# Kernel tuning notes

Hardware: AMD Instinct MI355X
Metric: run time of the kernel (lower is better)

Reference implementation:

```python
import jax, jax.numpy as jnp
import numpy as np

B, T, D = 2, 2048, 1024
N_HEADS, N_KV_HEADS = 16, 4
D_HEAD = D // N_HEADS            # 64
N_GROUPS = N_HEADS // N_KV_HEADS  # 4
ROPE_THETA = 10000.0


def _rope_freqs(t, d_head, theta):
    inv = 1.0 / (theta ** (jnp.arange(0, d_head, 2, dtype=jnp.float32) / d_head))  # (d_head/2,)
    ang = jnp.arange(t, dtype=jnp.float32)[:, None] * inv[None, :]                 # (T, d_head/2)
    return jnp.stack([jnp.cos(ang), jnp.sin(ang)], axis=-1)                        # (T, d_head/2, 2)


def _apply_rope(x, freqs):
    # x: (B, T, H, d_head); freqs: (T, d_head/2, 2) = (cos, sin)
    xr = x.reshape(*x.shape[:-1], -1, 2)          # (B,T,H,d/2,2)
    xre, xim = xr[..., 0], xr[..., 1]
    fre = freqs[None, :, None, :, 0]              # (1,T,1,d/2)
    fim = freqs[None, :, None, :, 1]
    outre = xre * fre - xim * fim
    outim = xre * fim + xim * fre
    return jnp.stack([outre, outim], axis=-1).reshape(x.shape)


def setup_inputs() -> dict:
    key = jax.random.key(0)
    ks = jax.random.split(key, 5)
    x = jax.random.normal(ks[0], (B, T, D), dtype=jnp.float32)
    w_q = jax.random.normal(ks[1], (N_HEADS * D_HEAD, D), dtype=jnp.float32) * 0.02
    w_k = jax.random.normal(ks[2], (N_KV_HEADS * D_HEAD, D), dtype=jnp.float32) * 0.02
    w_v = jax.random.normal(ks[3], (N_KV_HEADS * D_HEAD, D), dtype=jnp.float32) * 0.02
    w_o = jax.random.normal(ks[4], (D, N_HEADS * D_HEAD), dtype=jnp.float32) * 0.02
    rope_freqs = _rope_freqs(T, D_HEAD, ROPE_THETA)
    causal = jnp.tril(jnp.ones((T, T), dtype=bool))
    mask = jnp.where(causal, 0.0, -1e9).astype(jnp.float32)[None, None]  # (1,1,T,T)
    return {"x": x, "rope_freqs": rope_freqs, "mask": mask,
            "w_q": w_q, "w_k": w_k, "w_v": w_v, "w_o": w_o}


def reference(x, rope_freqs, mask, w_q, w_k, w_v, w_o):
    # projections (torch Linear: y = x @ W.T)
    q = jnp.einsum('btd,od->bto', x, w_q).reshape(B, T, N_HEADS, D_HEAD)
    k = jnp.einsum('btd,od->bto', x, w_k).reshape(B, T, N_KV_HEADS, D_HEAD)
    v = jnp.einsum('btd,od->bto', x, w_v).reshape(B, T, N_KV_HEADS, D_HEAD)
    q = _apply_rope(q, rope_freqs)
    k = _apply_rope(k, rope_freqs)
    # GQA: expand KV heads (kv head h -> N_GROUPS contiguous query heads)
    k = jnp.repeat(k, N_GROUPS, axis=2)   # (B,T,H,d)
    v = jnp.repeat(v, N_GROUPS, axis=2)
    q = q.transpose(0, 2, 1, 3)           # (B,H,T,d)
    k = k.transpose(0, 2, 1, 3)
    v = v.transpose(0, 2, 1, 3)
    scale = 1.0 / np.sqrt(D_HEAD).astype(np.float32)
    scores = jnp.einsum('bhqd,bhkd->bhqk', q, k) * scale + mask
    attn = jax.nn.softmax(scores, axis=-1)
    out = jnp.einsum('bhqk,bhkd->bhqd', attn, v)
    out = out.transpose(0, 2, 1, 3).reshape(B, T, N_HEADS * D_HEAD)
    return jnp.einsum('bto,do->btd', out, w_o)
```

## Files before the change

kernel.cpp:

```cpp
#include <hip/hip_runtime.h>
#include <hip/hip_bf16.h>
#include <cstddef>

#define TT   2048
#define NH   16
#define NKV  4
#define DH   64

typedef __bf16 bf16x8 __attribute__((ext_vector_type(8)));
typedef float  f32x4  __attribute__((ext_vector_type(4)));

#if __has_builtin(__builtin_amdgcn_exp2f)
#define EXP2F(x) __builtin_amdgcn_exp2f(x)
#else
#define EXP2F(x) __expf((x) * 0.69314718056f)
#endif

#define QSCALE 0.180336880f

__global__ __launch_bounds__(256)
void cast_kernel(const float* __restrict__ x,  const float* __restrict__ wq,
                 const float* __restrict__ wk, const float* __restrict__ wv,
                 const float* __restrict__ wo,
                 __bf16* __restrict__ xb, __bf16* __restrict__ wqkv,
                 __bf16* __restrict__ wob)
{
    const int g = blockIdx.x * 256 + threadIdx.x;
    const float* src;
    __bf16* dst;
    int off;
    if (g < 1048576)       { src = x;  dst = xb;   off = g; }
    else if (g < 1310720)  { src = wq; dst = wqkv; off = g - 1048576; }
    else if (g < 1376256)  { src = wk; dst = wqkv + 1048576; off = g - 1310720; }
    else if (g < 1441792)  { src = wv; dst = wqkv + 1310720; off = g - 1376256; }
    else                   { src = wo; dst = wob;  off = g - 1441792; }
    const float4 v = *(const float4*)(src + (size_t)off * 4);
    union { __bf16 h[4]; uint2 u; } o;
    o.h[0] = (__bf16)v.x; o.h[1] = (__bf16)v.y;
    o.h[2] = (__bf16)v.z; o.h[3] = (__bf16)v.w;
    *(uint2*)(dst + (size_t)off * 4) = o.u;
}

template<int MODE>
__global__ __launch_bounds__(128, 2)
void mm_kernel(const __bf16* __restrict__ A,
               const __bf16* __restrict__ W,
               const float* __restrict__ rope,
               void* __restrict__ O0, void* __restrict__ O1,
               void* __restrict__ O2)
{
    constexpr int K  = 1024;
    constexpr int NK = K / 32;
    __shared__ __bf16 As[64 * 32];
    __shared__ __bf16 Bs[128 * 32];

    const int tid  = threadIdx.x;
    const int lane = tid & 63;
    const int wv   = tid >> 6;
    const int quad = lane >> 4;
    const int lc   = lane & 15;
    const int gm0  = blockIdx.y * 64;
    const int gn0  = blockIdx.x * 128;
    const int wc0  = wv * 64;

    size_t gaA[2], gaB[4];
    int lsA[2], lsB[4];
#pragma unroll
    for (int j = 0; j < 2; j++) {
        const int p = tid + j * 128;
        const int r = p >> 2, q = (p & 3) ^ ((r >> 1) & 3);
        gaA[j] = (size_t)r * K + q * 8;
        lsA[j] = p * 8;
    }
#pragma unroll
    for (int j = 0; j < 4; j++) {
        const int p = tid + j * 128;
        const int r = p >> 2, q = (p & 3) ^ ((r >> 1) & 3);
        gaB[j] = (size_t)r * K + q * 8;
        lsB[j] = p * 8;
    }
    const __bf16* Ag = A + (size_t)gm0 * K;
    const __bf16* Wg = W + (size_t)gn0 * K;

    auto foff = [&](int row) { return (row * 4 + (quad ^ ((row >> 1) & 3))) * 8; };
    int aoff[4], boff[4];
#pragma unroll
    for (int i = 0; i < 4; i++) {
        aoff[i] = foff(i * 16 + lc);
        boff[i] = foff(wc0 + i * 16 + lc);
    }

    f32x4 acc[4][4];
#pragma unroll
    for (int i = 0; i < 4; i++)
#pragma unroll
        for (int j = 0; j < 4; j++) acc[i][j] = (f32x4){0.f, 0.f, 0.f, 0.f};

    bf16x8 ar[2], br[4];
    auto load_regs = [&](int kt) {
        const int kb = kt * 32;
#pragma unroll
        for (int j = 0; j < 2; j++) ar[j] = *(const bf16x8*)(Ag + gaA[j] + kb);
#pragma unroll
        for (int j = 0; j < 4; j++) br[j] = *(const bf16x8*)(Wg + gaB[j] + kb);
    };
    auto store_lds = [&]() {
#pragma unroll
        for (int j = 0; j < 2; j++) *(bf16x8*)&As[lsA[j]] = ar[j];
#pragma unroll
        for (int j = 0; j < 4; j++) *(bf16x8*)&Bs[lsB[j]] = br[j];
    };

    load_regs(0);
    store_lds();
    load_regs(1);
    __syncthreads();

    for (int kt = 0; kt < NK; kt++) {
        bf16x8 af[4], bfr[4];
#pragma unroll
        for (int i = 0; i < 4; i++) af[i]  = *(const bf16x8*)&As[aoff[i]];
#pragma unroll
        for (int j = 0; j < 4; j++) bfr[j] = *(const bf16x8*)&Bs[boff[j]];
#pragma unroll
        for (int i = 0; i < 4; i++)
#pragma unroll
            for (int j = 0; j < 4; j++)
                acc[i][j] = __builtin_amdgcn_mfma_f32_16x16x32_bf16(
                    af[i], bfr[j], acc[i][j], 0, 0, 0);

        if (kt + 1 < NK) {
            __syncthreads();
            store_lds();
            if (kt + 2 < NK) load_regs(kt + 2);
            __syncthreads();
        }
    }

    if (MODE == 0) {
        __bf16* Qo = (__bf16*)O0;
        __bf16* Ko = (__bf16*)O1;
        __bf16* Vo = (__bf16*)O2;
        const int region = (gn0 < 1024) ? 0 : (gn0 < 1280) ? 1 : 2;
#pragma unroll
        for (int i = 0; i < 4; i++) {
#pragma unroll
            for (int r = 0; r < 4; r++) {
                const int grow = gm0 + i * 16 + quad * 4 + r;
                const int b = grow >> 11, t = grow & 2047;
                const float* rrow = rope + t * 64;
#pragma unroll
                for (int j = 0; j < 4; j++) {
                    const float v = acc[i][j][r];
                    const float partner = __shfl_xor(v, 1, 64);
                    const int col = gn0 + wc0 + j * 16 + lc;
                    if (region == 0) {
                        const int h = col >> 6, d = col & 63;
                        const float2 cs = *(const float2*)(rrow + (d >> 1) * 2);
                        const float out = v * cs.x + partner * ((d & 1) ? cs.y : -cs.y);
                        Qo[((size_t)(b * NH + h) * TT + t) * DH + d] = (__bf16)(out * QSCALE);
                    } else if (region == 1) {
                        const int ck = col - 1024;
                        const int kh = ck >> 6, d = ck & 63;
                        const float2 cs = *(const float2*)(rrow + (d >> 1) * 2);
                        const float out = v * cs.x + partner * ((d & 1) ? cs.y : -cs.y);
                        Ko[((size_t)(b * NKV + kh) * TT + t) * DH + d] = (__bf16)out;
                    } else {
                        const int cv = col - 1280;
                        const int kh = cv >> 6, d = cv & 63;
                        Vo[((size_t)(b * NKV + kh) * DH + d) * TT + t] = (__bf16)v;
                    }
                }
            }
        }
    } else {
        float* Of = (float*)O0;
#pragma unroll
        for (int i = 0; i < 4; i++)
#pragma unroll
            for (int r = 0; r < 4; r++) {
                const int grow = gm0 + i * 16 + quad * 4 + r;
#pragma unroll
                for (int j = 0; j < 4; j++)
                    Of[(size_t)grow * 1024 + gn0 + wc0 + j * 16 + lc] = acc[i][j][r];
            }
    }
}

__global__ __launch_bounds__(128, 2)
void attn_kernel(const __bf16* __restrict__ Q,
                 const __bf16* __restrict__ K,
                 const __bf16* __restrict__ Vt,
                 __bf16* __restrict__ O)
{
    __shared__ __bf16 Ks[64 * 64];
    __shared__ __bf16 Vs[64 * 64];
    __shared__ __bf16 Ps[2][32][72];

    const int tid  = threadIdx.x;
    const int lane = tid & 63;
    const int wv   = tid >> 6;
    const int quad = lane >> 4;
    const int lc   = lane & 15;

    const int a   = blockIdx.x & 31;
    const int rep = blockIdx.x >> 5;
    const int qt  = ((rep >> 3) & 1) ? (31 - a) : a;
    const int b   = rep >> 4;
    const int h   = rep & 15;
    const int kh  = h >> 2;
    const int nk  = qt + 1;

    const __bf16* Kg = K  + (size_t)(b * NKV + kh) * TT * DH;
    const __bf16* Vg = Vt + (size_t)(b * NKV + kh) * DH * TT;

    bf16x8 qb[2][2];
#pragma unroll
    for (int u = 0; u < 2; u++) {
        const __bf16* qp = Q + ((size_t)(b * NH + h) * TT
                                + qt * 64 + wv * 32 + u * 16 + lc) * DH;
        qb[u][0] = *(const bf16x8*)(qp + quad * 8);
        qb[u][1] = *(const bf16x8*)(qp + 32 + quad * 8);
    }

    int koff[4], voff[4], lsl[4];
#pragma unroll
    for (int j = 0; j < 4; j++) {
        const int p  = tid + j * 128;
        const int r  = p >> 3;
        const int qs = (p & 7) ^ (r & 7);
        koff[j] = r * DH + qs * 8;
        voff[j] = r * TT + qs * 8;
        lsl[j]  = p * 8;
    }

    int foff[4][2];
#pragma unroll
    for (int g = 0; g < 4; g++)
#pragma unroll
        for (int c = 0; c < 2; c++)
            foff[g][c] = ((g * 16 + lc) * 8 + ((c * 4 + quad) ^ (lc & 7))) * 8;

    float l_s[2] = {0.f, 0.f};
    f32x4 oacc[2][4];
#pragma unroll
    for (int u = 0; u < 2; u++)
#pragma unroll
        for (int g = 0; g < 4; g++) oacc[u][g] = (f32x4){0.f, 0.f, 0.f, 0.f};

    bf16x8 kr[4], vr[4];
    auto load_regs = [&](int kt) {
        const __bf16* kp = Kg + (size_t)kt * 64 * DH;
        const __bf16* vp = Vg + (size_t)kt * 64;
#pragma unroll
        for (int j = 0; j < 4; j++) {
            kr[j] = *(const bf16x8*)(kp + koff[j]);
            vr[j] = *(const bf16x8*)(vp + voff[j]);
        }
    };
    auto store_lds = [&]() {
#pragma unroll
        for (int j = 0; j < 4; j++) {
            *(bf16x8*)&Ks[lsl[j]] = kr[j];
            *(bf16x8*)&Vs[lsl[j]] = vr[j];
        }
    };

    load_regs(0);
    store_lds();
    if (nk > 1) load_regs(1);
    __syncthreads();

    for (int kt = 0; kt < nk; kt++) {
        bf16x8 ka[4][2];
#pragma unroll
        for (int g = 0; g < 4; g++) {
            ka[g][0] = *(const bf16x8*)&Ks[foff[g][0]];
            ka[g][1] = *(const bf16x8*)&Ks[foff[g][1]];
        }

        const int Dbase = qt * 64 + wv * 32 - kt * 64;

        f32x4 s[2][4];
#pragma unroll
        for (int u = 0; u < 2; u++)
#pragma unroll
            for (int g = 0; g < 4; g++) {
                f32x4 z = (f32x4){0.f, 0.f, 0.f, 0.f};
                z = __builtin_amdgcn_mfma_f32_16x16x32_bf16(ka[g][0], qb[u][0], z, 0, 0, 0);
                z = __builtin_amdgcn_mfma_f32_16x16x32_bf16(ka[g][1], qb[u][1], z, 0, 0, 0);
                s[u][g] = z;
            }

#pragma unroll
        for (int u = 0; u < 2; u++) {
            const int D = Dbase + u * 16;
            if (D < 63) {
                const int thr = D + lc;
#pragma unroll
                for (int g = 0; g < 4; g++)
#pragma unroll
                    for (int r = 0; r < 4; r++)
                        if (g * 16 + quad * 4 + r > thr) s[u][g][r] = -1e30f;
            }
        }

#pragma unroll
        for (int u = 0; u < 2; u++) {
            float rs = 0.f;
#pragma unroll
            for (int g = 0; g < 4; g++) {
#pragma unroll
                for (int r = 0; r < 4; r++) {
                    s[u][g][r] = EXP2F(s[u][g][r]);
                    rs += s[u][g][r];
                }
                union { __bf16 hh[4]; uint2 uu; } pk;
                pk.hh[0] = (__bf16)s[u][g][0]; pk.hh[1] = (__bf16)s[u][g][1];
                pk.hh[2] = (__bf16)s[u][g][2]; pk.hh[3] = (__bf16)s[u][g][3];
                *(uint2*)&Ps[wv][u * 16 + lc][g * 16 + quad * 4] = pk.uu;
            }
            l_s[u] += rs;
        }

        bf16x8 va[4][2];
#pragma unroll
        for (int g = 0; g < 4; g++) {
            va[g][0] = *(const bf16x8*)&Vs[foff[g][0]];
            va[g][1] = *(const bf16x8*)&Vs[foff[g][1]];
        }

#pragma unroll
        for (int u = 0; u < 2; u++) {
            const bf16x8 pb0 = *(const bf16x8*)&Ps[wv][u * 16 + lc][quad * 8];
            const bf16x8 pb1 = *(const bf16x8*)&Ps[wv][u * 16 + lc][32 + quad * 8];
#pragma unroll
            for (int g = 0; g < 4; g++) {
                oacc[u][g] = __builtin_amdgcn_mfma_f32_16x16x32_bf16(va[g][0], pb0, oacc[u][g], 0, 0, 0);
                oacc[u][g] = __builtin_amdgcn_mfma_f32_16x16x32_bf16(va[g][1], pb1, oacc[u][g], 0, 0, 0);
            }
        }

        if (kt + 1 < nk) {
            __syncthreads();
            store_lds();
            if (kt + 2 < nk) load_regs(kt + 2);
            __syncthreads();
        }
    }

#pragma unroll
    for (int u = 0; u < 2; u++) {
        float l = l_s[u];
        l += __shfl_xor(l, 16, 64);
        l += __shfl_xor(l, 32, 64);
        const float inv = 1.f / l;
        const int t = qt * 64 + wv * 32 + u * 16 + lc;
        __bf16* op = O + (size_t)(b * TT + t) * (NH * DH) + h * DH;
#pragma unroll
        for (int g = 0; g < 4; g++) {
            union { __bf16 hh[4]; uint2 uu; } pk;
            pk.hh[0] = (__bf16)(oacc[u][g][0] * inv);
            pk.hh[1] = (__bf16)(oacc[u][g][1] * inv);
            pk.hh[2] = (__bf16)(oacc[u][g][2] * inv);
            pk.hh[3] = (__bf16)(oacc[u][g][3] * inv);
            *(uint2*)(op + g * 16 + quad * 4) = pk.uu;
        }
    }
}

extern "C" void kernel_launch(void* const* d_in, const int* in_sizes, int n_in,
                              void* d_out, int out_size, void* d_ws, size_t ws_size,
                              hipStream_t stream)
{
    const float* x    = (const float*)d_in[0];
    const float* rope = (const float*)d_in[1];
    const float* w_q  = (const float*)d_in[3];
    const float* w_k  = (const float*)d_in[4];
    const float* w_v  = (const float*)d_in[5];
    const float* w_o  = (const float*)d_in[6];
    float* out = (float*)d_out;

    char* ws = (char*)d_ws;
    __bf16* Qb   = (__bf16*)(ws);
    __bf16* Kb   = (__bf16*)(ws + (8  << 20));
    __bf16* Vtb  = (__bf16*)(ws + (10 << 20));
    __bf16* AOb  = (__bf16*)(ws + (12 << 20));
    __bf16* xb   = (__bf16*)(ws + (20 << 20));
    __bf16* Wqkv = (__bf16*)(ws + (28 << 20));
    __bf16* Wob  = (__bf16*)(ws + (31 << 20));

    cast_kernel<<<6656, dim3(256), 0, stream>>>(x, w_q, w_k, w_v, w_o,
                                                xb, Wqkv, Wob);

    dim3 g1(12, 64);
    mm_kernel<0><<<g1, dim3(128), 0, stream>>>(xb, Wqkv, rope,
                                               (void*)Qb, (void*)Kb, (void*)Vtb);

    attn_kernel<<<1024, dim3(128), 0, stream>>>(Qb, Kb, Vtb, AOb);

    dim3 g3(8, 64);
    mm_kernel<1><<<g3, dim3(128), 0, stream>>>(AOb, Wob, rope,
                                               (void*)out, nullptr, nullptr);
}
```

Baseline: 187.6 us.

## Double-buffer LDS tiles in GEMM and prefetch three k-steps ahead

Converts the projection GEMM main loop from a single LDS buffer with two barriers per k-step to ping-pong LDS buffers with one barrier per step. Register prefetch is deepened to two staged register sets, so global loads are issued three tiles ahead. This is meant to overlap global latency and LDS writes with MFMA work and halve barrier stalls. The cost is doubled LDS use (24KB) and more VGPRs, which may reduce occupancy under the (128,2) launch bound.

```diff
diff --git a/kernel.cpp b/kernel.cpp
--- a/kernel.cpp
+++ b/kernel.cpp
@@ -1,6 +1,7 @@
 #include <hip/hip_runtime.h>
 #include <hip/hip_bf16.h>
 #include <cstddef>
+#include <type_traits>
 
 #define TT   2048
 #define NH   16
@@ -51,8 +52,8 @@
 {
     constexpr int K  = 1024;
     constexpr int NK = K / 32;
-    __shared__ __bf16 As[64 * 32];
-    __shared__ __bf16 Bs[128 * 32];
+    __shared__ __bf16 As[2][64 * 32];
+    __shared__ __bf16 Bs[2][128 * 32];
 
     const int tid  = threadIdx.x;
     const int lane = tid & 63;
@@ -96,45 +97,58 @@
 #pragma unroll
         for (int j = 0; j < 4; j++) acc[i][j] = (f32x4){0.f, 0.f, 0.f, 0.f};
 
-    bf16x8 ar[2], br[4];
-    auto load_regs = [&](int kt) {
-        const int kb = kt * 32;
-#pragma unroll
-        for (int j = 0; j < 2; j++) ar[j] = *(const bf16x8*)(Ag + gaA[j] + kb);
-#pragma unroll
-        for (int j = 0; j < 4; j++) br[j] = *(const bf16x8*)(Wg + gaB[j] + kb);
-    };
-    auto store_lds = [&]() {
-#pragma unroll
-        for (int j = 0; j < 2; j++) *(bf16x8*)&As[lsA[j]] = ar[j];
-#pragma unroll
-        for (int j = 0; j < 4; j++) *(bf16x8*)&Bs[lsB[j]] = br[j];
-    };
-
-    load_regs(0);
-    store_lds();
-    load_regs(1);
+    bf16x8 ar[2][2], br[2][4];
+
+#pragma unroll
+    for (int j = 0; j < 2; j++) ar[0][j] = *(const bf16x8*)(Ag + gaA[j]);
+#pragma unroll
+    for (int j = 0; j < 4; j++) br[0][j] = *(const bf16x8*)(Wg + gaB[j]);
+#pragma unroll
+    for (int j = 0; j < 2; j++) *(bf16x8*)&As[0][lsA[j]] = ar[0][j];
+#pragma unroll
+    for (int j = 0; j < 4; j++) *(bf16x8*)&Bs[0][lsB[j]] = br[0][j];
+#pragma unroll
+    for (int j = 0; j < 2; j++) ar[1][j] = *(const bf16x8*)(Ag + gaA[j] + 32);
+#pragma unroll
+    for (int j = 0; j < 4; j++) br[1][j] = *(const bf16x8*)(Wg + gaB[j] + 32);
+#pragma unroll
+    for (int j = 0; j < 2; j++) ar[0][j] = *(const bf16x8*)(Ag + gaA[j] + 64);
+#pragma unroll
+    for (int j = 0; j < 4; j++) br[0][j] = *(const bf16x8*)(Wg + gaB[j] + 64);
     __syncthreads();
 
-    for (int kt = 0; kt < NK; kt++) {
+    auto step = [&](int kt, auto pc) {
+        constexpr int P = decltype(pc)::value;
+        constexpr int Q = 1 - P;
         bf16x8 af[4], bfr[4];
 #pragma unroll
-        for (int i = 0; i < 4; i++) af[i]  = *(const bf16x8*)&As[aoff[i]];
-#pragma unroll
-        for (int j = 0; j < 4; j++) bfr[j] = *(const bf16x8*)&Bs[boff[j]];
+        for (int i = 0; i < 4; i++) af[i]  = *(const bf16x8*)&As[P][aoff[i]];
+#pragma unroll
+        for (int j = 0; j < 4; j++) bfr[j] = *(const bf16x8*)&Bs[P][boff[j]];
+        if (kt + 1 < NK) {
+#pragma unroll
+            for (int j = 0; j < 2; j++) *(bf16x8*)&As[Q][lsA[j]] = ar[Q][j];
+#pragma unroll
+            for (int j = 0; j < 4; j++) *(bf16x8*)&Bs[Q][lsB[j]] = br[Q][j];
+        }
 #pragma unroll
         for (int i = 0; i < 4; i++)
 #pragma unroll
             for (int j = 0; j < 4; j++)
                 acc[i][j] = __builtin_amdgcn_mfma_f32_16x16x32_bf16(
                     af[i], bfr[j], acc[i][j], 0, 0, 0);
-
-        if (kt + 1 < NK) {
-            __syncthreads();
-            store_lds();
-            if (kt + 2 < NK) load_regs(kt + 2);
-            __syncthreads();
-        }
+        if (kt + 3 < NK) {
+            const int kb = (kt + 3) * 32;
+#pragma unroll
+            for (int j = 0; j < 2; j++) ar[Q][j] = *(const bf16x8*)(Ag + gaA[j] + kb);
+#pragma unroll
+            for (int j = 0; j < 4; j++) br[Q][j] = *(const bf16x8*)(Wg + gaB[j] + kb);
+        }
+        if (kt + 1 < NK) __syncthreads();
+    };
+    for (int kt = 0; kt < NK; kt += 2) {
+        step(kt,     std::integral_constant<int, 0>{});
+        step(kt + 1, std::integral_constant<int, 1>{});
     }
 
     if (MODE == 0) {
```

After: 185.7 us. About the same (-1.0%).
